# Optimization experiments

Measured on AMD Instinct MI355X. Metric: run time of the kernel, lower is better.

The kernel has to match this reference:

```python
import jax, jax.numpy as jnp
import numpy as np

SCALES = [128, 64, 32, 16]
EPS = 1e-12  # F.normalize default eps


def _nearest_resize(mask, sc):
    # mask: [B, N, H, W] bool -> [B, N, sc, sc] via nearest-neighbor subsampling
    H = mask.shape[-2]
    W = mask.shape[-1]
    ih = (jnp.arange(sc) * H) // sc
    iw = (jnp.arange(sc) * W) // sc
    return mask[:, :, ih][:, :, :, iw]


def _l2n(x):
    # normalize along last axis, matching F.normalize(p=2, eps=1e-12)
    n = jnp.linalg.norm(x, axis=-1, keepdims=True)
    return x / jnp.maximum(n, EPS)


def _sat_loss(olds, news, instance_mask):
    total = jnp.float32(0.0)
    for old, new, sc in zip(olds, news, SCALES):
        Bs, Heads, L, L1 = old.shape
        # permute(0,2,1,3).view(Bs,sc,sc,Heads,L1) == [Bs, L, Heads, L1]
        A_old = jnp.transpose(old, (0, 2, 1, 3))  # [B, L, H, K]
        A_new = jnp.transpose(new, (0, 2, 1, 3))
        m = _nearest_resize(instance_mask, sc).reshape(Bs, -1, L)  # [B, N, L]
        mf = m.astype(old.dtype)
        cnt = mf.sum(-1)[..., None, None]  # [B, N, 1, 1]
        # masked mean over spatial positions -> [B, N, H, K]
        mo = jnp.einsum('bnl,blhk->bnhk', mf, A_old) / cnt
        mn = jnp.einsum('bnl,blhk->bnhk', mf, A_new) / cnt
        d = jnp.linalg.norm(_l2n(mo) - _l2n(mn), axis=-1)  # [B, N, H]
        # mean over heads, instances, batch (all fixed sizes -> plain mean)
        total = total + d.mean()
    return total / len(SCALES)


def setup_inputs() -> dict:
    key = jax.random.key(0)
    ks = jax.random.split(key, 10)
    Bs, N, H, W = 2, 8, 512, 512
    shapes = [(Bs, 2, 16384, 256), (Bs, 3, 4096, 256), (Bs, 5, 1024, 256), (Bs, 8, 256, 256)]
    inp = {}
    for i, s in enumerate(shapes):
        inp[f'old{i}'] = jax.random.normal(ks[i], s, dtype=jnp.float32)
        inp[f'new{i}'] = jax.random.normal(ks[4 + i], s, dtype=jnp.float32)
    inp['instance_mask'] = jax.random.randint(ks[8], (Bs, N, H, W), 0, 2).astype(bool)
    inp['bbox'] = jax.random.uniform(ks[9], (Bs, N, 4), dtype=jnp.float32)
    return inp


def reference(old0, old1, old2, old3, new0, new1, new2, new3, instance_mask, bbox):
    # bbox is accepted but unused, as in the original forward
    return _sat_loss([old0, old1, old2, old3], [new0, new1, new2, new3], instance_mask)
```

## Files before the change

kernel.cpp:

```cpp
#include <hip/hip_runtime.h>


#define PACK0 0
#define PACK1 32768
#define PACK2 40960
#define PACK3 43008
#define CNT_OFF 43520
#define ACCO0 43584
#define ACCO1 51776
#define ACCO2 64064
#define ACCO3 84544
#define ACCN0 117312
#define ACCN1 125504
#define ACCN2 137792
#define ACCN3 158272
#define WS_END 191040
#define ZERO_WORDS (WS_END - CNT_OFF)
#define WS_BYTES ((size_t)WS_END * 4)

__device__ __forceinline__ int mask_mode(const unsigned char* __restrict__ mask)
{
    const unsigned* mu = (const unsigned*)mask;
    bool i32ok = true, f32ok = true;
#pragma unroll 8
    for (int j = 0; j < 64; ++j) {
        const unsigned d = mu[j];
        i32ok = i32ok && (d <= 1u);
        f32ok = f32ok && (d == 0u || d == 0x3F800000u);
    }
    return i32ok ? 1 : (f32ok ? 2 : 0);
}

__device__ __forceinline__ int mask_val(const unsigned char* __restrict__ mask,
                                        size_t e, int mode)
{
    if (mode == 0) return mask[e] != 0;
    if (mode == 1) return mask[e << 2] != 0;
    return mask[(e << 2) + 3] != 0;
}


__global__ __launch_bounds__(256) void zero_kernel(float* __restrict__ wsf,
                                                   float* __restrict__ out)
{
    const int tid = blockIdx.x * 256 + threadIdx.x;
    if (tid < ZERO_WORDS) wsf[CNT_OFF + tid] = 0.0f;
    if (tid == ZERO_WORDS) out[0] = 0.0f;
}

__global__ __launch_bounds__(256) void pack_kernel(
    const unsigned char* __restrict__ mask, unsigned* __restrict__ wsu,
    int* __restrict__ cnt)
{
    const int mode = mask_mode(mask);
    const int tid = blockIdx.x * 256 + threadIdx.x;
    int s, b, l, lsc, lstep, loff;
    if (tid < 32768)      { s = 0; b = tid >> 14; l = tid & 16383; lsc = 7; lstep = 2; loff = PACK0; }
    else if (tid < 40960) { int i2 = tid - 32768; s = 1; b = i2 >> 12; l = i2 & 4095; lsc = 6; lstep = 3; loff = PACK1; }
    else if (tid < 43008) { int i2 = tid - 40960; s = 2; b = i2 >> 10; l = i2 & 1023; lsc = 5; lstep = 4; loff = PACK2; }
    else                  { int i2 = tid - 43008; s = 3; b = i2 >> 8;  l = i2 & 255;  lsc = 4; lstep = 5; loff = PACK3; }

    const int y = l >> lsc;
    const int x = l & ((1 << lsc) - 1);
    const size_t base = (size_t)b * 2097152 + (size_t)(y << lstep) * 512 + (x << lstep);

    unsigned pm = 0;
#pragma unroll
    for (int q = 0; q < 8; ++q)
        pm |= (unsigned)mask_val(mask, base + (size_t)q * 262144, mode) << q;

    wsu[loff + (b << (2 * lsc)) + l] = pm;

#pragma unroll
    for (int q = 0; q < 8; ++q) {
        unsigned long long bal = __ballot((pm >> q) & 1u);
        if ((threadIdx.x & 63) == 0)
            atomicAdd(&cnt[s * 16 + b * 8 + q], (int)__popcll(bal));
    }
}

template <int Hs, int Ls, int CH, int CHUNKS, int PACKOFF, int ACCOOFF, int ACCNOFF>
__device__ __forceinline__ void scale_body(
    int i, const float* __restrict__ op, const float* __restrict__ np_,
    const unsigned* __restrict__ wsu, float* __restrict__ wsf, float4* red)
{
    const int t = threadIdx.x;
    const int r = t >> 6;
    const int c = t & 63;
    const int chunk = i % CHUNKS;
    const int bh = i / CHUNKS;
    const int b = bh / Hs;
    const int h = bh % Hs;

    const unsigned* pk = wsu + PACKOFF + b * Ls + chunk * CH;
    const size_t rowbase = ((size_t)(b * Hs + h) * Ls + (size_t)chunk * CH) * 256;
    const float* po = op + rowbase;
    const float* pn = np_ + rowbase;

    float4 ao[8], an[8];
#pragma unroll
    for (int q = 0; q < 8; ++q) {
        ao[q] = make_float4(0.f, 0.f, 0.f, 0.f);
        an[q] = make_float4(0.f, 0.f, 0.f, 0.f);
    }

#pragma unroll 2
    for (int lb = 0; lb < CH; lb += 4) {
        const int l = lb + r;
        const unsigned pm = (unsigned)__builtin_amdgcn_readfirstlane((int)pk[l]);
        const float4 o = *(const float4*)(po + (size_t)l * 256 + c * 4);
        const float4 v = *(const float4*)(pn + (size_t)l * 256 + c * 4);
#pragma unroll
        for (int q = 0; q < 8; ++q) {
            if (pm & (1u << q)) {
                ao[q].x += o.x; ao[q].y += o.y; ao[q].z += o.z; ao[q].w += o.w;
                an[q].x += v.x; an[q].y += v.y; an[q].z += v.z; an[q].w += v.w;
            }
        }
    }

#pragma unroll
    for (int q = 0; q < 8; ++q) {
        red[t] = ao[q];
        __syncthreads();
        if (t < 64) {
            const float4 A = red[t], Bv = red[t + 64], Cv = red[t + 128], Dv = red[t + 192];
            float* dst = wsf + ACCOOFF + ((size_t)(b * 8 + q) * Hs + h) * 256 + t * 4;
            atomicAdd(dst + 0, A.x + Bv.x + Cv.x + Dv.x);
            atomicAdd(dst + 1, A.y + Bv.y + Cv.y + Dv.y);
            atomicAdd(dst + 2, A.z + Bv.z + Cv.z + Dv.z);
            atomicAdd(dst + 3, A.w + Bv.w + Cv.w + Dv.w);
        }
        __syncthreads();
        red[t] = an[q];
        __syncthreads();
        if (t < 64) {
            const float4 A = red[t], Bv = red[t + 64], Cv = red[t + 128], Dv = red[t + 192];
            float* dst = wsf + ACCNOFF + ((size_t)(b * 8 + q) * Hs + h) * 256 + t * 4;
            atomicAdd(dst + 0, A.x + Bv.x + Cv.x + Dv.x);
            atomicAdd(dst + 1, A.y + Bv.y + Cv.y + Dv.y);
            atomicAdd(dst + 2, A.z + Bv.z + Cv.z + Dv.z);
            atomicAdd(dst + 3, A.w + Bv.w + Cv.w + Dv.w);
        }
        __syncthreads();
    }
}

__global__ __launch_bounds__(256) void main_kernel(
    const float* __restrict__ o0, const float* __restrict__ o1,
    const float* __restrict__ o2, const float* __restrict__ o3,
    const float* __restrict__ q0, const float* __restrict__ q1,
    const float* __restrict__ q2, const float* __restrict__ q3,
    const unsigned* __restrict__ wsu, float* __restrict__ wsf)
{
    __shared__ float4 red[256];
    const int bid = blockIdx.x;
    if (bid < 512)       scale_body<2, 16384, 128, 128, PACK0, ACCO0, ACCN0>(bid,       o0, q0, wsu, wsf, red);
    else if (bid < 704)  scale_body<3,  4096, 128,  32, PACK1, ACCO1, ACCN1>(bid - 512, o1, q1, wsu, wsf, red);
    else if (bid < 784)  scale_body<5,  1024, 128,   8, PACK2, ACCO2, ACCN2>(bid - 704, o2, q2, wsu, wsf, red);
    else                 scale_body<8,   256,  64,   4, PACK3, ACCO3, ACCN3>(bid - 784, o3, q3, wsu, wsf, red);
}

__global__ __launch_bounds__(64) void finalize_kernel(
    const float* __restrict__ wsf, const int* __restrict__ cnt,
    float* __restrict__ out)
{
    const int bid = blockIdx.x;
    const int t = threadIdx.x;
    int s, H, i, acco, accn;
    if (bid < 32)       { s = 0; H = 2; i = bid;       acco = ACCO0; accn = ACCN0; }
    else if (bid < 80)  { s = 1; H = 3; i = bid - 32;  acco = ACCO1; accn = ACCN1; }
    else if (bid < 160) { s = 2; H = 5; i = bid - 80;  acco = ACCO2; accn = ACCN2; }
    else                { s = 3; H = 8; i = bid - 160; acco = ACCO3; accn = ACCN3; }
    const int h = i % H;
    const int bn = i / H;
    const int n = bn & 7;
    const int b = bn >> 3;

    const float cf = (float)cnt[s * 16 + b * 8 + n];
    const size_t off = ((size_t)(b * 8 + n) * H + h) * 256 + t * 4;
    const float4 so = *(const float4*)(wsf + acco + off);
    const float4 sn = *(const float4*)(wsf + accn + off);

    const float mox = so.x / cf, moy = so.y / cf, moz = so.z / cf, mow = so.w / cf;
    const float mnx = sn.x / cf, mny = sn.y / cf, mnz = sn.z / cf, mnw = sn.w / cf;

    float po = mox * mox + moy * moy + moz * moz + mow * mow;
    float pq = mnx * mnx + mny * mny + mnz * mnz + mnw * mnw;
#pragma unroll
    for (int m = 1; m < 64; m <<= 1) {
        po += __shfl_xor(po, m);
        pq += __shfl_xor(pq, m);
    }
    const float no = fmaxf(sqrtf(po), 1e-12f);
    const float nn = fmaxf(sqrtf(pq), 1e-12f);

    const float dx = mox / no - mnx / nn;
    const float dy = moy / no - mny / nn;
    const float dz = moz / no - mnz / nn;
    const float dw = mow / no - mnw / nn;
    float dd = dx * dx + dy * dy + dz * dz + dw * dw;
#pragma unroll
    for (int m = 1; m < 64; m <<= 1) dd += __shfl_xor(dd, m);

    if (t == 0)
        atomicAdd(out, sqrtf(dd) * (0.25f / (16.0f * (float)H)));
}


__global__ __launch_bounds__(64) void fb_zero_out(float* __restrict__ out)
{
    if (threadIdx.x == 0) out[0] = 0.0f;
}

template <int SC, int LSC, int LSTEP, int Hs>
__device__ __forceinline__ void fb_body(
    int b, int h, const float* __restrict__ op, const float* __restrict__ np_,
    const unsigned char* __restrict__ mask, float* __restrict__ out,
    unsigned char* pmLds, float4* red, int* scnt)
{
    const int t = threadIdx.x;
    constexpr int L = SC * SC;
    const int mode = mask_mode(mask);

    if (t < 8) scnt[t] = 0;
    __syncthreads();

    int pcnt[8];
#pragma unroll
    for (int q = 0; q < 8; ++q) pcnt[q] = 0;
    for (int l = t; l < L; l += 512) {
        const int y = l >> LSC;
        const int x = l & (SC - 1);
        const size_t base = (size_t)b * 2097152 + (size_t)(y << LSTEP) * 512 + (x << LSTEP);
        unsigned pm = 0;
#pragma unroll
        for (int q = 0; q < 8; ++q) {
            const int v = mask_val(mask, base + (size_t)q * 262144, mode);
            pm |= (unsigned)v << q;
            pcnt[q] += v;
        }
        pmLds[l] = (unsigned char)pm;
    }
#pragma unroll
    for (int q = 0; q < 8; ++q) {
        int v = pcnt[q];
#pragma unroll
        for (int m = 1; m < 64; m <<= 1) v += __shfl_xor(v, m);
        if ((t & 63) == 0) atomicAdd(&scnt[q], v);
    }
    __syncthreads();

    const int r = t >> 6;
    const int c = t & 63;
    float4 ao[8], an[8];
#pragma unroll
    for (int q = 0; q < 8; ++q) {
        ao[q] = make_float4(0.f, 0.f, 0.f, 0.f);
        an[q] = make_float4(0.f, 0.f, 0.f, 0.f);
    }
    const size_t rowbase = (size_t)(b * Hs + h) * L * 256;
    for (int lb = 0; lb < L; lb += 8) {
        const int l = lb + r;
        const unsigned pm = pmLds[l];
        const float4 o = *(const float4*)(op + rowbase + (size_t)l * 256 + c * 4);
        const float4 v = *(const float4*)(np_ + rowbase + (size_t)l * 256 + c * 4);
#pragma unroll
        for (int q = 0; q < 8; ++q) {
            if (pm & (1u << q)) {
                ao[q].x += o.x; ao[q].y += o.y; ao[q].z += o.z; ao[q].w += o.w;
                an[q].x += v.x; an[q].y += v.y; an[q].z += v.z; an[q].w += v.w;
            }
        }
    }
    __syncthreads();

#pragma unroll
    for (int q = 0; q < 8; ++q) {
        float mox = 0.f, moy = 0.f, moz = 0.f, mow = 0.f;
        float mnx = 0.f, mny = 0.f, mnz = 0.f, mnw = 0.f;
        red[t] = ao[q];
        __syncthreads();
        if (t < 64) {
            float4 s = make_float4(0.f, 0.f, 0.f, 0.f);
#pragma unroll
            for (int w = 0; w < 8; ++w) {
                const float4 A = red[t + 64 * w];
                s.x += A.x; s.y += A.y; s.z += A.z; s.w += A.w;
            }
            const float inv = 1.0f / (float)scnt[q];
            mox = s.x * inv; moy = s.y * inv; moz = s.z * inv; mow = s.w * inv;
        }
        __syncthreads();
        red[t] = an[q];
        __syncthreads();
        if (t < 64) {
            float4 s = make_float4(0.f, 0.f, 0.f, 0.f);
#pragma unroll
            for (int w = 0; w < 8; ++w) {
                const float4 A = red[t + 64 * w];
                s.x += A.x; s.y += A.y; s.z += A.z; s.w += A.w;
            }
            const float inv = 1.0f / (float)scnt[q];
            mnx = s.x * inv; mny = s.y * inv; mnz = s.z * inv; mnw = s.w * inv;

            float po = mox * mox + moy * moy + moz * moz + mow * mow;
            float pn2 = mnx * mnx + mny * mny + mnz * mnz + mnw * mnw;
#pragma unroll
            for (int m = 1; m < 64; m <<= 1) {
                po  += __shfl_xor(po, m);
                pn2 += __shfl_xor(pn2, m);
            }
            const float no = fmaxf(sqrtf(po), 1e-12f);
            const float nn = fmaxf(sqrtf(pn2), 1e-12f);
            const float dx = mox / no - mnx / nn;
            const float dy = moy / no - mny / nn;
            const float dz = moz / no - mnz / nn;
            const float dw = mow / no - mnw / nn;
            float dd = dx * dx + dy * dy + dz * dz + dw * dw;
#pragma unroll
            for (int m = 1; m < 64; m <<= 1) dd += __shfl_xor(dd, m);
            if (t == 0)
                atomicAdd(out, sqrtf(dd) * (0.25f / (16.0f * (float)Hs)));
        }
        __syncthreads();
    }
}

__global__ __launch_bounds__(512) void fb_kernel(
    const float* __restrict__ o0, const float* __restrict__ o1,
    const float* __restrict__ o2, const float* __restrict__ o3,
    const float* __restrict__ q0, const float* __restrict__ q1,
    const float* __restrict__ q2, const float* __restrict__ q3,
    const unsigned char* __restrict__ mask, float* __restrict__ out)
{
    __shared__ unsigned char pmLds[16384];
    __shared__ float4 red[512];
    __shared__ int scnt[8];
    const int bid = blockIdx.x;
    if (bid < 4)        fb_body<128, 7, 2, 2>(bid >> 1, bid & 1, o0, q0, mask, out, pmLds, red, scnt);
    else if (bid < 10) { const int i = bid - 4;  fb_body<64, 6, 3, 3>(i / 3, i % 3, o1, q1, mask, out, pmLds, red, scnt); }
    else if (bid < 20) { const int i = bid - 10; fb_body<32, 5, 4, 5>(i / 5, i % 5, o2, q2, mask, out, pmLds, red, scnt); }
    else               { const int i = bid - 20; fb_body<16, 4, 5, 8>(i / 8, i % 8, o3, q3, mask, out, pmLds, red, scnt); }
}

extern "C" void kernel_launch(void* const* d_in, const int* in_sizes, int n_in,
                              void* d_out, int out_size, void* d_ws, size_t ws_size,
                              hipStream_t stream)
{
    const float* olds[4] = {nullptr, nullptr, nullptr, nullptr};
    const float* news[4] = {nullptr, nullptr, nullptr, nullptr};
    const unsigned char* mask = nullptr;
    for (int i = 0; i < n_in; ++i) {
        const long long sz = in_sizes[i];
        int s = -1;
        if (sz == 16777216)      s = 0;
        else if (sz == 6291456)  s = 1;
        else if (sz == 2621440)  s = 2;
        else if (sz == 1048576)  s = 3;
        else if (sz == 4194304) { mask = (const unsigned char*)d_in[i]; continue; }
        else continue;
        if (!olds[s]) olds[s] = (const float*)d_in[i];
        else if (!news[s]) news[s] = (const float*)d_in[i];
    }

    if (!mask || !olds[0] || !news[0] || !olds[1] || !news[1] ||
        !olds[2] || !news[2] || !olds[3] || !news[3]) {
        fb_zero_out<<<1, 64, 0, stream>>>((float*)d_out);
        return;
    }

    if (ws_size >= WS_BYTES && d_ws != nullptr) {
        unsigned* wsu = (unsigned*)d_ws;
        float* wsf = (float*)d_ws;
        int* cnt = (int*)d_ws + CNT_OFF;
        zero_kernel<<<577, 256, 0, stream>>>(wsf, (float*)d_out);
        pack_kernel<<<170, 256, 0, stream>>>(mask, wsu, cnt);
        main_kernel<<<848, 256, 0, stream>>>(olds[0], olds[1], olds[2], olds[3],
                                             news[0], news[1], news[2], news[3],
                                             wsu, wsf);
        finalize_kernel<<<288, 64, 0, stream>>>(wsf, cnt, (float*)d_out);
    } else {
        fb_zero_out<<<1, 64, 0, stream>>>((float*)d_out);
        fb_kernel<<<36, 512, 0, stream>>>(olds[0], olds[1], olds[2], olds[3],
                                          news[0], news[1], news[2], news[3],
                                          mask, (float*)d_out);
    }
}
```

Measured before the change: 332.1 us.

## Replace float atomics with private per-block partials and widen mask packing

The main kernel now writes each block's per-instance partial sums to a private workspace slot, and the finalize kernel reduces over the chunks. This replaces global float atomics into shared accumulators and removes the large zeroing pass. The mask pack kernel spreads the 8 instance lookups across lanes and packs the bits with a ballot into one byte per position. The mask-mode check becomes a single wave vote, and the branchy masked accumulate becomes branchless FMAs. The cost is a much larger workspace requirement and extra finalize reads, with a fallback to the atomic path when the workspace is smaller.

```diff
diff --git a/kernel.cpp b/kernel.cpp
--- a/kernel.cpp
+++ b/kernel.cpp
@@ -1,33 +1,32 @@
 #include <hip/hip_runtime.h>
 
 
-#define PACK0 0
-#define PACK1 32768
-#define PACK2 40960
-#define PACK3 43008
-#define CNT_OFF 43520
-#define ACCO0 43584
-#define ACCO1 51776
-#define ACCO2 64064
-#define ACCO3 84544
-#define ACCN0 117312
-#define ACCN1 125504
-#define ACCN2 137792
-#define ACCN3 158272
-#define WS_END 191040
-#define ZERO_WORDS (WS_END - CNT_OFF)
-#define WS_BYTES ((size_t)WS_END * 4)
-
-__device__ __forceinline__ int mask_mode(const unsigned char* __restrict__ mask)
+#define CNT_OFF 10880
+#define PART0W 10944
+#define PART1W 2108096
+#define PART2W 2894528
+#define PART3W 3222208
+#define WS_PRIV_WORDS 3484352
+#define WS_PRIV_BYTES ((size_t)WS_PRIV_WORDS * 4)
+
+#define ACCO0 10944
+#define ACCO1 19136
+#define ACCO2 31424
+#define ACCO3 51904
+#define ACCN0 84672
+#define ACCN1 92864
+#define ACCN2 105152
+#define ACCN3 125440
+#define WS_ATOM_WORDS 158400
+#define WS_ATOM_BYTES ((size_t)WS_ATOM_WORDS * 4)
+#define ZERO_WORDS (WS_ATOM_WORDS - CNT_OFF)
+
+__device__ __forceinline__ int mask_mode_wave(const unsigned char* __restrict__ mask)
 {
     const unsigned* mu = (const unsigned*)mask;
-    bool i32ok = true, f32ok = true;
-#pragma unroll 8
-    for (int j = 0; j < 64; ++j) {
-        const unsigned d = mu[j];
-        i32ok = i32ok && (d <= 1u);
-        f32ok = f32ok && (d == 0u || d == 0x3F800000u);
-    }
+    const unsigned d = mu[threadIdx.x & 63];
+    const int i32ok = __all(d <= 1u);
+    const int f32ok = __all(d == 0u || d == 0x3F800000u);
     return i32ok ? 1 : (f32ok ? 2 : 0);
 }
 
@@ -40,49 +39,64 @@
 }
 
 
-__global__ __launch_bounds__(256) void zero_kernel(float* __restrict__ wsf,
-                                                   float* __restrict__ out)
+__global__ __launch_bounds__(256) void zero_atom(float* __restrict__ wsf,
+                                                 float* __restrict__ out)
 {
     const int tid = blockIdx.x * 256 + threadIdx.x;
     if (tid < ZERO_WORDS) wsf[CNT_OFF + tid] = 0.0f;
     if (tid == ZERO_WORDS) out[0] = 0.0f;
 }
 
+__global__ __launch_bounds__(128) void zero_priv(float* __restrict__ wsf,
+                                                 float* __restrict__ out)
+{
+    const int t = threadIdx.x;
+    if (t < 64) wsf[CNT_OFF + t] = 0.0f;
+    if (t == 64) out[0] = 0.0f;
+}
+
+__global__ __launch_bounds__(64) void fb_zero_out(float* __restrict__ out)
+{
+    if (threadIdx.x == 0) out[0] = 0.0f;
+}
+
 __global__ __launch_bounds__(256) void pack_kernel(
-    const unsigned char* __restrict__ mask, unsigned* __restrict__ wsu,
+    const unsigned char* __restrict__ mask, unsigned char* __restrict__ pmB,
     int* __restrict__ cnt)
 {
-    const int mode = mask_mode(mask);
+    const int mode = mask_mode_wave(mask);
     const int tid = blockIdx.x * 256 + threadIdx.x;
-    int s, b, l, lsc, lstep, loff;
-    if (tid < 32768)      { s = 0; b = tid >> 14; l = tid & 16383; lsc = 7; lstep = 2; loff = PACK0; }
-    else if (tid < 40960) { int i2 = tid - 32768; s = 1; b = i2 >> 12; l = i2 & 4095; lsc = 6; lstep = 3; loff = PACK1; }
-    else if (tid < 43008) { int i2 = tid - 40960; s = 2; b = i2 >> 10; l = i2 & 1023; lsc = 5; lstep = 4; loff = PACK2; }
-    else                  { int i2 = tid - 43008; s = 3; b = i2 >> 8;  l = i2 & 255;  lsc = 4; lstep = 5; loff = PACK3; }
+    const int lane = tid & 63;
+    const int g = lane >> 3;
+    const int q = lane & 7;
+    const int item = (tid >> 6) * 8 + g;
+
+    int s, b, l, lsc, lstep;
+    if (item < 32768)      { s = 0; b = item >> 14; l = item & 16383; lsc = 7; lstep = 2; }
+    else if (item < 40960) { int j = item - 32768; s = 1; b = j >> 12; l = j & 4095; lsc = 6; lstep = 3; }
+    else if (item < 43008) { int j = item - 40960; s = 2; b = j >> 10; l = j & 1023; lsc = 5; lstep = 4; }
+    else                   { int j = item - 43008; s = 3; b = j >> 8;  l = j & 255;  lsc = 4; lstep = 5; }
 
     const int y = l >> lsc;
     const int x = l & ((1 << lsc) - 1);
-    const size_t base = (size_t)b * 2097152 + (size_t)(y << lstep) * 512 + (x << lstep);
-
-    unsigned pm = 0;
-#pragma unroll
-    for (int q = 0; q < 8; ++q)
-        pm |= (unsigned)mask_val(mask, base + (size_t)q * 262144, mode) << q;
-
-    wsu[loff + (b << (2 * lsc)) + l] = pm;
-
-#pragma unroll
-    for (int q = 0; q < 8; ++q) {
-        unsigned long long bal = __ballot((pm >> q) & 1u);
-        if ((threadIdx.x & 63) == 0)
-            atomicAdd(&cnt[s * 16 + b * 8 + q], (int)__popcll(bal));
-    }
-}
-
-template <int Hs, int Ls, int CH, int CHUNKS, int PACKOFF, int ACCOOFF, int ACCNOFF>
+    const size_t e = (size_t)b * 2097152 + (size_t)(y << lstep) * 512 + (x << lstep)
+                   + (size_t)q * 262144;
+    const int v = mask_val(mask, e, mode);
+
+    const unsigned long long bal = __ballot(v);
+    if (q == 0)
+        pmB[item] = (unsigned char)((bal >> (g * 8)) & 0xFFull);
+    if (g == 0) {
+        const int c = (int)__popcll(bal & (0x0101010101010101ull << q));
+        atomicAdd(&cnt[s * 16 + b * 8 + q], c);
+    }
+}
+
+template <int Hs, int Ls, int CH, int CHUNKS, int PB, int PRIVW,
+          int ACCO, int ACCN, bool PRIV>
 __device__ __forceinline__ void scale_body(
     int i, const float* __restrict__ op, const float* __restrict__ np_,
-    const unsigned* __restrict__ wsu, float* __restrict__ wsf, float4* red)
+    const unsigned char* __restrict__ pmB, float* __restrict__ wsf, float4* red)
 {
     const int t = threadIdx.x;
     const int r = t >> 6;
@@ -92,7 +106,7 @@
     const int b = bh / Hs;
     const int h = bh % Hs;
 
-    const unsigned* pk = wsu + PACKOFF + b * Ls + chunk * CH;
+    const unsigned char* pk = pmB + PB + b * Ls + chunk * CH;
     const size_t rowbase = ((size_t)(b * Hs + h) * Ls + (size_t)chunk * CH) * 256;
     const float* po = op + rowbase;
     const float* pn = np_ + rowbase;
@@ -107,15 +121,20 @@
 #pragma unroll 2
     for (int lb = 0; lb < CH; lb += 4) {
         const int l = lb + r;
-        const unsigned pm = (unsigned)__builtin_amdgcn_readfirstlane((int)pk[l]);
+        const unsigned pm = pk[l];
         const float4 o = *(const float4*)(po + (size_t)l * 256 + c * 4);
         const float4 v = *(const float4*)(pn + (size_t)l * 256 + c * 4);
 #pragma unroll
         for (int q = 0; q < 8; ++q) {
-            if (pm & (1u << q)) {
-                ao[q].x += o.x; ao[q].y += o.y; ao[q].z += o.z; ao[q].w += o.w;
-                an[q].x += v.x; an[q].y += v.y; an[q].z += v.z; an[q].w += v.w;
-            }
+            const float m = (float)((pm >> q) & 1u);
+            ao[q].x = fmaf(o.x, m, ao[q].x);
+            ao[q].y = fmaf(o.y, m, ao[q].y);
+            ao[q].z = fmaf(o.z, m, ao[q].z);
+            ao[q].w = fmaf(o.w, m, ao[q].w);
+            an[q].x = fmaf(v.x, m, an[q].x);
+            an[q].y = fmaf(v.y, m, an[q].y);
+            an[q].z = fmaf(v.z, m, an[q].z);
+            an[q].w = fmaf(v.w, m, an[q].w);
         }
     }
 
@@ -125,63 +144,89 @@
         __syncthreads();
         if (t < 64) {
             const float4 A = red[t], Bv = red[t + 64], Cv = red[t + 128], Dv = red[t + 192];
-            float* dst = wsf + ACCOOFF + ((size_t)(b * 8 + q) * Hs + h) * 256 + t * 4;
-            atomicAdd(dst + 0, A.x + Bv.x + Cv.x + Dv.x);
-            atomicAdd(dst + 1, A.y + Bv.y + Cv.y + Dv.y);
-            atomicAdd(dst + 2, A.z + Bv.z + Cv.z + Dv.z);
-            atomicAdd(dst + 3, A.w + Bv.w + Cv.w + Dv.w);
+            const float4 s4 = make_float4(A.x + Bv.x + Cv.x + Dv.x,
+                                          A.y + Bv.y + Cv.y + Dv.y,
+                                          A.z + Bv.z + Cv.z + Dv.z,
+                                          A.w + Bv.w + Cv.w + Dv.w);
+            if (PRIV) {
+                *(float4*)(wsf + PRIVW + (size_t)i * 4096 + q * 256 + t * 4) = s4;
+            } else {
+                float* dst = wsf + ACCO + ((size_t)(b * 8 + q) * Hs + h) * 256 + t * 4;
+                atomicAdd(dst + 0, s4.x); atomicAdd(dst + 1, s4.y);
+                atomicAdd(dst + 2, s4.z); atomicAdd(dst + 3, s4.w);
+            }
         }
         __syncthreads();
         red[t] = an[q];
         __syncthreads();
         if (t < 64) {
             const float4 A = red[t], Bv = red[t + 64], Cv = red[t + 128], Dv = red[t + 192];
-            float* dst = wsf + ACCNOFF + ((size_t)(b * 8 + q) * Hs + h) * 256 + t * 4;
-            atomicAdd(dst + 0, A.x + Bv.x + Cv.x + Dv.x);
-            atomicAdd(dst + 1, A.y + Bv.y + Cv.y + Dv.y);
-            atomicAdd(dst + 2, A.z + Bv.z + Cv.z + Dv.z);
-            atomicAdd(dst + 3, A.w + Bv.w + Cv.w + Dv.w);
-        }
-        __syncthreads();
-    }
-}
-
-__global__ __launch_bounds__(256) void main_kernel(
+            const float4 s4 = make_float4(A.x + Bv.x + Cv.x + Dv.x,
+                                          A.y + Bv.y + Cv.y + Dv.y,
+                                          A.z + Bv.z + Cv.z + Dv.z,
+                                          A.w + Bv.w + Cv.w + Dv.w);
+            if (PRIV) {
+                *(float4*)(wsf + PRIVW + (size_t)i * 4096 + 2048 + q * 256 + t * 4) = s4;
+            } else {
+                float* dst = wsf + ACCN + ((size_t)(b * 8 + q) * Hs + h) * 256 + t * 4;
+                atomicAdd(dst + 0, s4.x); atomicAdd(dst + 1, s4.y);
+                atomicAdd(dst + 2, s4.z); atomicAdd(dst + 3, s4.w);
+            }
+        }
+        __syncthreads();
+    }
+}
+
+template <bool PRIV>
+__global__ __launch_bounds__(256, 4) void main_kernel(
     const float* __restrict__ o0, const float* __restrict__ o1,
     const float* __restrict__ o2, const float* __restrict__ o3,
     const float* __restrict__ q0, const float* __restrict__ q1,
     const float* __restrict__ q2, const float* __restrict__ q3,
-    const unsigned* __restrict__ wsu, float* __restrict__ wsf)
+    const unsigned char* __restrict__ pmB, float* __restrict__ wsf)
 {
     __shared__ float4 red[256];
     const int bid = blockIdx.x;
-    if (bid < 512)       scale_body<2, 16384, 128, 128, PACK0, ACCO0, ACCN0>(bid,       o0, q0, wsu, wsf, red);
-    else if (bid < 704)  scale_body<3,  4096, 128,  32, PACK1, ACCO1, ACCN1>(bid - 512, o1, q1, wsu, wsf, red);
-    else if (bid < 784)  scale_body<5,  1024, 128,   8, PACK2, ACCO2, ACCN2>(bid - 704, o2, q2, wsu, wsf, red);
-    else                 scale_body<8,   256,  64,   4, PACK3, ACCO3, ACCN3>(bid - 784, o3, q3, wsu, wsf, red);
-}
-
-__global__ __launch_bounds__(64) void finalize_kernel(
-    const float* __restrict__ wsf, const int* __restrict__ cnt,
+    if (bid < 512)
+        scale_body<2, 16384, 128, 128, 0,     PART0W, ACCO0, ACCN0, PRIV>(bid,       o0, q0, pmB, wsf, red);
+    else if (bid < 704)
+        scale_body<3, 4096,  128, 32,  32768, PART1W, ACCO1, ACCN1, PRIV>(bid - 512, o1, q1, pmB, wsf, red);
+    else if (bid < 784)
+        scale_body<5, 1024,  128, 8,   40960, PART2W, ACCO2, ACCN2, PRIV>(bid - 704, o2, q2, pmB, wsf, red);
+    else
+        scale_body<8, 256,   64,  4,   43008, PART3W, ACCO3, ACCN3, PRIV>(bid - 784, o3, q3, pmB, wsf, red);
+}
+
+template <int Hs, int CHUNKS, int PRIVW, int ACCO, int ACCN, bool PRIV>
+__device__ __forceinline__ void fin_body(
+    int s, int i, const float* __restrict__ wsf, const int* __restrict__ cnt,
     float* __restrict__ out)
 {
-    const int bid = blockIdx.x;
     const int t = threadIdx.x;
-    int s, H, i, acco, accn;
-    if (bid < 32)       { s = 0; H = 2; i = bid;       acco = ACCO0; accn = ACCN0; }
-    else if (bid < 80)  { s = 1; H = 3; i = bid - 32;  acco = ACCO1; accn = ACCN1; }
-    else if (bid < 160) { s = 2; H = 5; i = bid - 80;  acco = ACCO2; accn = ACCN2; }
-    else                { s = 3; H = 8; i = bid - 160; acco = ACCO3; accn = ACCN3; }
-    const int h = i % H;
-    const int bn = i / H;
+    const int h = i % Hs;
+    const int bn = i / Hs;
     const int n = bn & 7;
     const int b = bn >> 3;
 
+    float4 so = make_float4(0.f, 0.f, 0.f, 0.f);
+    float4 sn = make_float4(0.f, 0.f, 0.f, 0.f);
+    if (PRIV) {
+        const int bh = b * Hs + h;
+#pragma unroll 4
+        for (int ch = 0; ch < CHUNKS; ++ch) {
+            const size_t base = PRIVW + ((size_t)bh * CHUNKS + ch) * 4096 + n * 256 + t * 4;
+            const float4 A = *(const float4*)(wsf + base);
+            const float4 Bv = *(const float4*)(wsf + base + 2048);
+            so.x += A.x;  so.y += A.y;  so.z += A.z;  so.w += A.w;
+            sn.x += Bv.x; sn.y += Bv.y; sn.z += Bv.z; sn.w += Bv.w;
+        }
+    } else {
+        const size_t off = ((size_t)(b * 8 + n) * Hs + h) * 256 + t * 4;
+        so = *(const float4*)(wsf + ACCO + off);
+        sn = *(const float4*)(wsf + ACCN + off);
+    }
+
     const float cf = (float)cnt[s * 16 + b * 8 + n];
-    const size_t off = ((size_t)(b * 8 + n) * H + h) * 256 + t * 4;
-    const float4 so = *(const float4*)(wsf + acco + off);
-    const float4 sn = *(const float4*)(wsf + accn + off);
-
     const float mox = so.x / cf, moy = so.y / cf, moz = so.z / cf, mow = so.w / cf;
     const float mnx = sn.x / cf, mny = sn.y / cf, mnz = sn.z / cf, mnw = sn.w / cf;
 
@@ -204,13 +249,19 @@
     for (int m = 1; m < 64; m <<= 1) dd += __shfl_xor(dd, m);
 
     if (t == 0)
-        atomicAdd(out, sqrtf(dd) * (0.25f / (16.0f * (float)H)));
-}
-
-
-__global__ __launch_bounds__(64) void fb_zero_out(float* __restrict__ out)
-{
-    if (threadIdx.x == 0) out[0] = 0.0f;
+        atomicAdd(out, sqrtf(dd) * (0.25f / (16.0f * (float)Hs)));
+}
+
+template <bool PRIV>
+__global__ __launch_bounds__(64) void finalize_kernel(
+    const float* __restrict__ wsf, const int* __restrict__ cnt,
+    float* __restrict__ out)
+{
+    const int bid = blockIdx.x;
+    if (bid < 32)       fin_body<2, 128, PART0W, ACCO0, ACCN0, PRIV>(0, bid,       wsf, cnt, out);
+    else if (bid < 80)  fin_body<3, 32,  PART1W, ACCO1, ACCN1, PRIV>(1, bid - 32,  wsf, cnt, out);
+    else if (bid < 160) fin_body<5, 8,   PART2W, ACCO2, ACCN2, PRIV>(2, bid - 80,  wsf, cnt, out);
+    else                fin_body<8, 4,   PART3W, ACCO3, ACCN3, PRIV>(3, bid - 160, wsf, cnt, out);
 }
 
 template <int SC, int LSC, int LSTEP, int Hs>
@@ -221,7 +272,7 @@
 {
     const int t = threadIdx.x;
     constexpr int L = SC * SC;
-    const int mode = mask_mode(mask);
+    const int mode = mask_mode_wave(mask);
 
     if (t < 8) scnt[t] = 0;
     __syncthreads();
@@ -267,10 +318,11 @@
         const float4 v = *(const float4*)(np_ + rowbase + (size_t)l * 256 + c * 4);
 #pragma unroll
         for (int q = 0; q < 8; ++q) {
-            if (pm & (1u << q)) {
-                ao[q].x += o.x; ao[q].y += o.y; ao[q].z += o.z; ao[q].w += o.w;
-                an[q].x += v.x; an[q].y += v.y; an[q].z += v.z; an[q].w += v.w;
-            }
+            const float m = (float)((pm >> q) & 1u);
+            ao[q].x = fmaf(o.x, m, ao[q].x); ao[q].y = fmaf(o.y, m, ao[q].y);
+            ao[q].z = fmaf(o.z, m, ao[q].z); ao[q].w = fmaf(o.w, m, ao[q].w);
+            an[q].x = fmaf(v.x, m, an[q].x); an[q].y = fmaf(v.y, m, an[q].y);
+            an[q].z = fmaf(v.z, m, an[q].z); an[q].w = fmaf(v.w, m, an[q].w);
         }
     }
     __syncthreads();
@@ -370,16 +422,24 @@
         return;
     }
 
-    if (ws_size >= WS_BYTES && d_ws != nullptr) {
-        unsigned* wsu = (unsigned*)d_ws;
-        float* wsf = (float*)d_ws;
-        int* cnt = (int*)d_ws + CNT_OFF;
-        zero_kernel<<<577, 256, 0, stream>>>(wsf, (float*)d_out);
-        pack_kernel<<<170, 256, 0, stream>>>(mask, wsu, cnt);
-        main_kernel<<<848, 256, 0, stream>>>(olds[0], olds[1], olds[2], olds[3],
-                                             news[0], news[1], news[2], news[3],
-                                             wsu, wsf);
-        finalize_kernel<<<288, 64, 0, stream>>>(wsf, cnt, (float*)d_out);
+    float* wsf = (float*)d_ws;
+    unsigned char* pmB = (unsigned char*)d_ws;
+    int* cnt = (int*)d_ws + CNT_OFF;
+
+    if (ws_size >= WS_PRIV_BYTES && d_ws != nullptr) {
+        zero_priv<<<1, 128, 0, stream>>>(wsf, (float*)d_out);
+        pack_kernel<<<1360, 256, 0, stream>>>(mask, pmB, cnt);
+        main_kernel<true><<<848, 256, 0, stream>>>(olds[0], olds[1], olds[2], olds[3],
+                                                   news[0], news[1], news[2], news[3],
+                                                   pmB, wsf);
+        finalize_kernel<true><<<288, 64, 0, stream>>>(wsf, cnt, (float*)d_out);
+    } else if (ws_size >= WS_ATOM_BYTES && d_ws != nullptr) {
+        zero_atom<<<577, 256, 0, stream>>>(wsf, (float*)d_out);
+        pack_kernel<<<1360, 256, 0, stream>>>(mask, pmB, cnt);
+        main_kernel<false><<<848, 256, 0, stream>>>(olds[0], olds[1], olds[2], olds[3],
+                                                    news[0], news[1], news[2], news[3],
+                                                    pmB, wsf);
+        finalize_kernel<false><<<288, 64, 0, stream>>>(wsf, cnt, (float*)d_out);
     } else {
         fb_zero_out<<<1, 64, 0, stream>>>((float*)d_out);
         fb_kernel<<<36, 512, 0, stream>>>(olds[0], olds[1], olds[2], olds[3],
```

Measured after the change: 309.0 us. -6.9%, faster.
